# Kernel optimization log

Hardware: AMD Instinct MI355X
Metric: run time of the kernel (lower is better)

## Reference

```python
import jax, jax.numpy as jnp
import numpy as np

N = 8192      # nodes
DIN = 128     # in_channels
DH = 64       # hidden_channels (dim_out, num_heads=1)
DOUT = 32     # out_channels
RATIO = 0.5
K_KEEP = int(np.ceil(RATIO * N))  # SAGPooling keep count (single graph)
LN_EPS = 1e-5


def _linear_params(k, fan_in, fan_out):
    kw, kb = jax.random.split(k)
    W = jax.random.normal(kw, (fan_in, fan_out), dtype=jnp.float32) / jnp.sqrt(jnp.float32(fan_in))
    b = jax.random.normal(kb, (fan_out,), dtype=jnp.float32) * 0.01
    return W, b


def setup_inputs() -> dict:
    key = jax.random.key(0)
    ks = jax.random.split(key, 8)
    x = jax.random.normal(ks[0], (N, DIN), dtype=jnp.float32)
    batch = jnp.zeros((N,), dtype=jnp.int64)  # single graph
    Wq, bq = _linear_params(ks[1], DIN, DH)
    Wk, bk = _linear_params(ks[2], DIN, DH)
    Wv, bv = _linear_params(ks[3], DIN, DH)
    gcn_W, gcn_b = _linear_params(ks[4], DH, DH)       # GCNConv weight/bias
    score_W, score_b = _linear_params(ks[5], DH, 1)    # SAGPooling score GCNConv
    ln_g = jnp.ones((DH,), dtype=jnp.float32)
    ln_b = jnp.zeros((DH,), dtype=jnp.float32)
    head_W, head_b = _linear_params(ks[6], DH, DOUT)
    return dict(x=x, batch=batch, Wq=Wq, bq=bq, Wk=Wk, bk=bk, Wv=Wv, bv=bv,
                gcn_W=gcn_W, gcn_b=gcn_b, score_W=score_W, score_b=score_b,
                ln_g=ln_g, ln_b=ln_b, head_W=head_W, head_b=head_b)


def _forward(x, Wq, bq, Wk, bk, Wv, bv, gcn_W, gcn_b, score_W, score_b,
             ln_g, ln_b, head_W, head_b):
    # --- self-attention over all nodes (num_heads = 1) ---
    Q = x @ Wq + bq                                        # [N, DH]
    K = x @ Wk + bk
    V = x @ Wv + bv
    attn = jax.nn.softmax(Q @ K.T / jnp.sqrt(jnp.float32(DH)), axis=-1)  # [N, N]
    h = attn @ V                                           # [N, DH]

    # --- edge construction: threshold attention, ensure self-loops ---
    # (attn > 0.5).nonzero() -> edge set; empty -> self-loop fallback; then
    # add_self_loops. Dense equivalent: A = max(mask, I).
    eye = jnp.eye(N, dtype=x.dtype)
    A = jnp.maximum((attn > 0.5).astype(x.dtype), eye)     # [N, N], diag = 1

    # symmetric GCN normalization  D^{-1/2} A D^{-1/2}
    dinv = jax.lax.rsqrt(A.sum(axis=1))                    # [N]
    An = dinv[:, None] * A * dinv[None, :]                 # [N, N]

    # --- GCNConv layer ---
    g = An @ (h @ gcn_W) + gcn_b                           # [N, DH]

    # --- SAGPooling: GCNConv scorer -> tanh -> global top-k (single graph) ---
    score = jnp.tanh((An @ (g @ score_W) + score_b).squeeze(-1))  # [N]
    top_scores, perm = jax.lax.top_k(score, K_KEEP)        # sorted desc, like PyG topk
    xp = g[perm] * top_scores[:, None]                     # [K, DH], multiplier = 1

    # --- LayerNorm + ReLU (dropout is identity in eval) ---
    mu = xp.mean(axis=-1, keepdims=True)
    var = xp.var(axis=-1, keepdims=True)
    xp = (xp - mu) * jax.lax.rsqrt(var + LN_EPS) * ln_g + ln_b
    xp = jax.nn.relu(xp)

    # --- prediction head ---
    return xp @ head_W + head_b                            # [K, DOUT]


def reference(x, batch, Wq, bq, Wk, bk, Wv, bv, gcn_W, gcn_b,
              score_W, score_b, ln_g, ln_b, head_W, head_b):
    del batch  # single graph; grouping has no effect on the math
    return _forward(x, Wq, bq, Wk, bk, Wv, bv, gcn_W, gcn_b,
                    score_W, score_b, ln_g, ln_b, head_W, head_b)
```

## Files before the change

kernel.cpp:

```cpp
#include <hip/hip_runtime.h>
#include <hip/hip_bf16.h>
#include <cstdio>

typedef __hip_bfloat16 bf16;
typedef __attribute__((ext_vector_type(8))) short v8s;
typedef __attribute__((ext_vector_type(4))) short v4s;
typedef __attribute__((ext_vector_type(4))) float v4f;
typedef __attribute__((ext_vector_type(4))) double v4d;

#define MFMA16(a, b, c) __builtin_amdgcn_mfma_f32_16x16x32_bf16((a), (b), (c), 0, 0, 0)

#define NN 8192
#define DIN 128
#define DH 64
#define DOUT 32
#define KKEEP 4096
#define SPLITS 16
#define SPATT 16
#define RS2 0.70710678118654752440

__device__ __forceinline__ float bf2f(bf16 v) { return __bfloat162float(v); }
__device__ __forceinline__ short f2bfs(float f) {
  __hip_bfloat16 h = __float2bfloat16(f);
  return *reinterpret_cast<short*>(&h);
}
__device__ __forceinline__ bf16 f2bf(float v) { return __float2bfloat16(v); }

__device__ __forceinline__ double exp_d(double s) {
  const double L2E    = 1.4426950408889634074;
  const double LN2_HI = 6.93147180369123816490e-01;
  const double LN2_LO = 1.90821492927058770002e-10;
  double t  = s * L2E;
  double kf = rint(t);
  double r  = fma(-kf, LN2_HI, s);
  r = fma(-kf, LN2_LO, r);
  double p = 1.0 / 362880.0;
  p = fma(p, r, 1.0 / 40320.0);
  p = fma(p, r, 1.0 / 5040.0);
  p = fma(p, r, 1.0 / 720.0);
  p = fma(p, r, 1.0 / 120.0);
  p = fma(p, r, 1.0 / 24.0);
  p = fma(p, r, 1.0 / 6.0);
  p = fma(p, r, 0.5);
  p = fma(p, r, 1.0);
  p = fma(p, r, 1.0);
  int k = (int)kf;
  long long bits = ((long long)(1023 + k)) << 52;
  double sc = __longlong_as_double(bits);
  return p * sc;
}

__global__ __launch_bounds__(256) void k1_prep(
    const float* __restrict__ x, const float* __restrict__ Wq, const float* __restrict__ bq,
    const float* __restrict__ Wk, const float* __restrict__ bk, const float* __restrict__ Wv,
    const float* __restrict__ bv, const float* __restrict__ gW, const float* __restrict__ sW,
    double* __restrict__ Qd, double* __restrict__ Kd, double* __restrict__ w,
    bf16* __restrict__ Qb, bf16* __restrict__ Kb, bf16* __restrict__ Vt) {
  __shared__ double xs[16][DIN];
  int t = threadIdx.x;
  int nb = blockIdx.x * 16;
  for (int idx = t; idx < 16 * DIN; idx += 256)
    xs[idx >> 7][idx & 127] = (double)x[(size_t)nb * DIN + idx];
  __syncthreads();
  int d = t & 63;
  int sub = t >> 6;
  double ud = 0.0;
  for (int dd = 0; dd < DH; ++dd) ud = fma((double)gW[d * DH + dd], (double)sW[dd], ud);
  double bqd = (double)bq[d];
  double bkd = (double)bk[d];
  double bvd = (double)bv[d];
  for (int pass = 0; pass < 4; ++pass) {
    int n = pass * 4 + sub;
    double aq = bqd, ak = bkd, av = bvd;
#pragma unroll 8
    for (int c = 0; c < DIN; ++c) {
      double xv = xs[n][c];
      aq = fma(xv, (double)Wq[c * DH + d], aq);
      ak = fma(xv, (double)Wk[c * DH + d], ak);
      av = fma(xv, (double)Wv[c * DH + d], av);
    }
    aq *= 0.125;
    int node = nb + n;
    Qd[(size_t)node * DH + d] = aq;
    Kd[(size_t)node * DH + d] = ak;
    Qb[(size_t)node * DH + d] = f2bf((float)aq);
    Kb[(size_t)node * DH + d] = f2bf((float)ak);
    Vt[(size_t)d * NN + node] = f2bf((float)av);
    double pw = av * ud;
#pragma unroll
    for (int off = 32; off; off >>= 1) pw += __shfl_xor(pw, off);
    if (d == 0) w[node] = pw;
  }
}

__global__ __launch_bounds__(256) void k24_seq(
    const double* __restrict__ Qd, const double* __restrict__ Kd, const double* __restrict__ w,
    double* __restrict__ Zp, double* __restrict__ Wp, double* __restrict__ Ep, int* __restrict__ Jp,
    const bf16* __restrict__ Qb, const bf16* __restrict__ Kb, const bf16* __restrict__ Vt,
    float* __restrict__ hp, float* __restrict__ zp) {
  __shared__ __align__(16) char smem[16896];
  const int t = threadIdx.x;
  const int wv = t >> 6;
  const int l = t & 63;

  {
    double (*Kbuf)[16][66] = (double (*)[16][66])smem;
    const int li = l & 15, lg = l >> 4;
    const int rb = (blockIdx.x & 127) * 64;
    const int sp = blockIdx.x >> 7;
    const int cbeg = sp * (NN / SPLITS);

    double qreg[16];
    const double* qrow = Qd + (size_t)(rb + 16 * wv + li) * DH + lg;
#pragma unroll
    for (int tt = 0; tt < 16; ++tt) qreg[tt] = qrow[4 * tt];

    {
      const double* src = Kd + (size_t)cbeg * DH;
      int r = t >> 4, c = (t & 15) * 4;
      *(double2*)&Kbuf[0][r][c]     = *(const double2*)&src[r * DH + c];
      *(double2*)&Kbuf[0][r][c + 2] = *(const double2*)&src[r * DH + c + 2];
    }
    __syncthreads();

    double Zt[4] = {0, 0, 0, 0}, Wt[4] = {0, 0, 0, 0}, Et[4] = {-1, -1, -1, -1};
    int Jt[4] = {0, 0, 0, 0};

    const int NT = (NN / SPLITS) / 16;
    for (int kt = 0; kt < NT; ++kt) {
      const int buf = kt & 1;
      if (kt + 1 < NT) {
        const double* src = Kd + (size_t)(cbeg + (kt + 1) * 16) * DH;
        int r = t >> 4, c = (t & 15) * 4;
        *(double2*)&Kbuf[buf ^ 1][r][c]     = *(const double2*)&src[r * DH + c];
        *(double2*)&Kbuf[buf ^ 1][r][c + 2] = *(const double2*)&src[r * DH + c + 2];
      }
      v4d acc = (v4d){0.0, 0.0, 0.0, 0.0};
      __builtin_amdgcn_s_setprio(1);
#pragma unroll
      for (int tt = 0; tt < 16; ++tt) {
        double bfrag = Kbuf[buf][li][4 * tt + lg];
        acc = __builtin_amdgcn_mfma_f64_16x16x4f64(qreg[tt], bfrag, acc, 0, 0, 0);
      }
      __builtin_amdgcn_s_setprio(0);
      const int col = cbeg + kt * 16 + li;
      const double wj = w[col];
#pragma unroll
      for (int v = 0; v < 4; ++v) {
        double e = exp_d(acc[v]);
        Zt[v] += e;
        Wt[v] = fma(e, wj, Wt[v]);
        if (e > Et[v]) { Et[v] = e; Jt[v] = col; }
      }
      __syncthreads();
    }

#pragma unroll
    for (int v = 0; v < 4; ++v) {
#pragma unroll
      for (int m = 1; m < 16; m <<= 1) {
        Zt[v] += __shfl_xor(Zt[v], m);
        Wt[v] += __shfl_xor(Wt[v], m);
        double e2 = __shfl_xor(Et[v], m);
        int j2 = __shfl_xor(Jt[v], m);
        if (e2 > Et[v] || (e2 == Et[v] && j2 < Jt[v])) { Et[v] = e2; Jt[v] = j2; }
      }
    }
    if (li == 0) {
#pragma unroll
      for (int v = 0; v < 4; ++v) {
        int row = rb + 16 * wv + lg + 4 * v;
        Zp[sp * NN + row] = Zt[v];
        Wp[sp * NN + row] = Wt[v];
        Ep[sp * NN + row] = Et[v];
        Jp[sp * NN + row] = Jt[v];
      }
    }
  }
  __syncthreads();

  {
    short (*P)[16 * 40] = (short (*)[16 * 40])smem;
    const int g = l >> 4, li = l & 15;
    const int qb = (blockIdx.x & 127) * 64 + wv * 16;
    const int sp = blockIdx.x >> 7;
    short* Pw = &P[wv][0];
    const v8s q0 = *(const v8s*)(Qb + (size_t)(qb + li) * DH + g * 8);
    const v8s q1 = *(const v8s*)(Qb + (size_t)(qb + li) * DH + 32 + g * 8);
    v4f hacc[4];
#pragma unroll
    for (int db = 0; db < 4; ++db) hacc[db] = (v4f){0.f, 0.f, 0.f, 0.f};
    float zl = 0.f;
    const int kbeg = sp * (NN / SPATT);
    for (int jb = kbeg; jb < kbeg + NN / SPATT; jb += 32) {
      const bf16* kp = Kb + (size_t)(jb + li) * DH + g * 8;
      v8s ka0 = *(const v8s*)(kp);
      v8s ka1 = *(const v8s*)(kp + 32);
      v8s kb0 = *(const v8s*)(kp + 16 * DH);
      v8s kb1 = *(const v8s*)(kp + 16 * DH + 32);
      v4f c0 = (v4f){0.f, 0.f, 0.f, 0.f}, c1 = (v4f){0.f, 0.f, 0.f, 0.f};
      __builtin_amdgcn_s_setprio(1);
      c0 = MFMA16(ka0, q0, c0);
      c0 = MFMA16(ka1, q1, c0);
      c1 = MFMA16(kb0, q0, c1);
      c1 = MFMA16(kb1, q1, c1);
      __builtin_amdgcn_s_setprio(0);
      v4s p0, p1;
#pragma unroll
      for (int r = 0; r < 4; ++r) {
        short b0 = f2bfs(__expf(c0[r]));
        short b1 = f2bfs(__expf(c1[r]));
        p0[r] = b0;
        p1[r] = b1;
        zl += bf2f(*reinterpret_cast<bf16*>(&b0));
        zl += bf2f(*reinterpret_cast<bf16*>(&b1));
      }
      *(v4s*)&Pw[li * 40 + g * 4] = p0;
      *(v4s*)&Pw[li * 40 + 16 + g * 4] = p1;
      v8s pf = *(const v8s*)&Pw[li * 40 + g * 8];
#pragma unroll
      for (int db = 0; db < 4; ++db) {
        const v8s vb = *(const v8s*)(Vt + (size_t)(db * 16 + li) * NN + jb + g * 8);
        hacc[db] = MFMA16(pf, vb, hacc[db]);
      }
    }
    zl += __shfl_xor(zl, 16);
    zl += __shfl_xor(zl, 32);
    if (g == 0) zp[sp * NN + qb + li] = zl;
#pragma unroll
    for (int r = 0; r < 4; ++r) {
      int row = qb + g * 4 + r;
#pragma unroll
      for (int db = 0; db < 4; ++db)
        hp[((size_t)sp * NN + row) * DH + db * 16 + li] = hacc[db][r];
    }
  }
}

__device__ __forceinline__ double tau_of(int k, const double* __restrict__ Zp,
                                         const double* __restrict__ Wp) {
  double Z = 0, W = 0;
  for (int sp = 0; sp < SPLITS; ++sp) { Z += Zp[sp * NN + k]; W += Wp[sp * NN + k]; }
  return W / Z;
}
__device__ __forceinline__ void exj_of(int k, const double* __restrict__ Zp,
                                       const double* __restrict__ Ep, const int* __restrict__ Jp,
                                       int& exo, int& jo) {
  double Z = 0, E = -1;
  int J = 0;
  for (int sp = 0; sp < SPLITS; ++sp) {
    Z += Zp[sp * NN + k];
    double e = Ep[sp * NN + k];
    if (e > E || (e == E && Jp[sp * NN + k] < J)) { E = e; J = Jp[sp * NN + k]; }
  }
  exo = (E > 0.5 * Z) && (J != k);
  jo = J & (NN - 1);
}
__device__ __forceinline__ double tarr_of(int k, const double* __restrict__ Zp,
                                          const double* __restrict__ Wp,
                                          const double* __restrict__ Ep,
                                          const int* __restrict__ Jp, double cb) {
  int exk, jk;
  exj_of(k, Zp, Ep, Jp, exk, jk);
  double dk = exk ? RS2 : 1.0;
  double acc = dk * tau_of(k, Zp, Wp);
  if (exk) {
    int exj, jj;
    exj_of(jk, Zp, Ep, Jp, exj, jj);
    double dj = exj ? RS2 : 1.0;
    acc = fma(dj, tau_of(jk, Zp, Wp), acc);
  }
  return fma(dk, acc, cb);
}

__global__ void k356(const double* __restrict__ Zp, const double* __restrict__ Wp,
                     const double* __restrict__ Ep, const int* __restrict__ Jp,
                     const float* __restrict__ gb, const float* __restrict__ sW,
                     const float* __restrict__ score_b,
                     int* __restrict__ ex_out, int* __restrict__ jm_out,
                     double* __restrict__ pre, float* __restrict__ sc32, int* __restrict__ cnt) {
  int i = blockIdx.x * 256 + threadIdx.x;
  double cb = 0.0;
  for (int d = 0; d < DH; ++d) cb = fma((double)gb[d], (double)sW[d], cb);
  int exi, ji;
  exj_of(i, Zp, Ep, Jp, exi, ji);
  ex_out[i] = exi;
  jm_out[i] = ji;
  double di = exi ? RS2 : 1.0;
  double acc = di * tarr_of(i, Zp, Wp, Ep, Jp, cb);
  if (exi) {
    int exj, jj;
    exj_of(ji, Zp, Ep, Jp, exj, jj);
    double dj = exj ? RS2 : 1.0;
    acc = fma(dj, tarr_of(ji, Zp, Wp, Ep, Jp, cb), acc);
  }
  double p = fma(di, acc, (double)score_b[0]);
  pre[i] = p;
  sc32[i] = (float)tanh(p);
  cnt[i] = 0;
}

__global__ __launch_bounds__(256) void k9_hM(const float* __restrict__ hp, const float* __restrict__ zp,
                                             const float* __restrict__ gW, float* __restrict__ M) {
  __shared__ float xs[4][DH];
  int t = threadIdx.x;
  int sub = t >> 6, d = t & 63;
  int n = blockIdx.x * 4 + sub;
  float Z = 0.f, H = 0.f;
#pragma unroll
  for (int sp = 0; sp < SPATT; ++sp) {
    Z += zp[sp * NN + n];
    H += hp[((size_t)sp * NN + n) * DH + d];
  }
  xs[sub][d] = H / Z;
  __syncthreads();
  float acc = 0.f;
#pragma unroll 8
  for (int c = 0; c < DH; ++c) acc = fmaf(xs[sub][c], gW[c * DH + d], acc);
  M[(size_t)n * DH + d] = acc;
}

__global__ void k7_rank(const double* __restrict__ pre, int* __restrict__ cnt) {
  __shared__ double pj[512];
  int i = (blockIdx.x & 31) * 256 + threadIdx.x;
  int j0 = (blockIdx.x >> 5) * 512;
  for (int k = threadIdx.x; k < 512; k += 256) pj[k] = pre[j0 + k];
  __syncthreads();
  double si = pre[i];
  int c = 0;
#pragma unroll 8
  for (int j = 0; j < 512; ++j) {
    double v = pj[j];
    c += (v > si || (v == si && (j0 + j) < i));
  }
  atomicAdd(&cnt[i], c);
}

__global__ void k8_sel(const int* __restrict__ cnt, int* __restrict__ sel) {
  int i = blockIdx.x * 256 + threadIdx.x;
  unsigned r = (unsigned)cnt[i];
  if (r < KKEEP) sel[r] = i;
}

__global__ __launch_bounds__(256) void k11_head(const float* __restrict__ M, const int* __restrict__ extra,
                                                const int* __restrict__ jmA, const float* __restrict__ gb,
                                                const float* __restrict__ sc32, const int* __restrict__ sel,
                                                const float* __restrict__ lg, const float* __restrict__ lb,
                                                const float* __restrict__ hW, const float* __restrict__ hb,
                                                float* __restrict__ out) {
  __shared__ float xs[4][DH];
  int t = threadIdx.x;
  int wv = t >> 6, d = t & 63;
  int p = blockIdx.x * 4 + wv;
  int i = sel[p] & (NN - 1);
  int ex = extra[i];
  float di = ex ? 0.70710678f : 1.0f;
  float acc0 = di * M[(size_t)i * DH + d];
  if (ex) {
    int j = jmA[i] & (NN - 1);
    acc0 = fmaf(extra[j] ? 0.70710678f : 1.0f, M[(size_t)j * DH + d], acc0);
  }
  float gval = fmaf(di, acc0, gb[d]);
  float v = gval * sc32[i];
  float s1 = v;
#pragma unroll
  for (int off = 32; off; off >>= 1) s1 += __shfl_xor(s1, off);
  float mu = s1 * (1.0f / 64.0f);
  float dv = v - mu;
  float s2 = dv * dv;
#pragma unroll
  for (int off = 32; off; off >>= 1) s2 += __shfl_xor(s2, off);
  float var = s2 * (1.0f / 64.0f);
  float xn = dv * rsqrtf(var + 1e-5f) * lg[d] + lb[d];
  xs[wv][d] = fmaxf(xn, 0.0f);
  __syncthreads();
  if (t < 128) {
    int r = t >> 5, o = t & 31;
    float acc = hb[o];
#pragma unroll 8
    for (int c = 0; c < DH; ++c) acc = fmaf(xs[r][c], hW[c * DOUT + o], acc);
    out[(size_t)(blockIdx.x * 4 + r) * DOUT + o] = acc;
  }
}

#define MB 1048576ull
constexpr size_t OFF_QD   = 0 * MB;
constexpr size_t OFF_KD   = 4 * MB;
constexpr size_t OFF_M    = 16 * MB;
constexpr size_t OFF_ZP   = 20 * MB;
constexpr size_t OFF_WP   = 21 * MB;
constexpr size_t OFF_EP   = 22 * MB;
constexpr size_t OFF_JP   = 23 * MB;
constexpr size_t OFF_W    = 24 * MB;
constexpr size_t OFF_EX   = 27 * MB;
constexpr size_t OFF_JM   = 28 * MB;
constexpr size_t OFF_PRE  = 30 * MB;
constexpr size_t OFF_SC   = 31 * MB;
constexpr size_t OFF_CNT  = 32 * MB;
constexpr size_t OFF_SEL  = 33 * MB;
constexpr size_t OFF_HP   = 34 * MB;
constexpr size_t OFF_ZATT = 66 * MB;
constexpr size_t OFF_QB   = 67 * MB;
constexpr size_t OFF_KB   = 68 * MB;
constexpr size_t OFF_VT   = 69 * MB;
constexpr size_t WS_NEEDED = 70 * MB;

extern "C" void kernel_launch(void* const* d_in, const int* in_sizes, int n_in,
                              void* d_out, int out_size, void* d_ws, size_t ws_size,
                              hipStream_t stream) {
  if (n_in < 16 || ws_size < WS_NEEDED || out_size != KKEEP * DOUT) {
    fprintf(stderr, "[sag] GUARD ws=%zu need=%zu n_in=%d out=%d\n", ws_size, WS_NEEDED, n_in, out_size);
    return;
  }
  const float* x   = (const float*)d_in[0];
  const float* Wq  = (const float*)d_in[2];
  const float* bq  = (const float*)d_in[3];
  const float* Wk  = (const float*)d_in[4];
  const float* bk  = (const float*)d_in[5];
  const float* Wv  = (const float*)d_in[6];
  const float* bv  = (const float*)d_in[7];
  const float* gW  = (const float*)d_in[8];
  const float* gb  = (const float*)d_in[9];
  const float* sW  = (const float*)d_in[10];
  const float* sb  = (const float*)d_in[11];
  const float* lg  = (const float*)d_in[12];
  const float* lb  = (const float*)d_in[13];
  const float* hW  = (const float*)d_in[14];
  const float* hb  = (const float*)d_in[15];
  float* out = (float*)d_out;

  char* ws = (char*)d_ws;
  double* Qd  = (double*)(ws + OFF_QD);
  double* Kd  = (double*)(ws + OFF_KD);
  bf16*   Qb  = (bf16*)(ws + OFF_QB);
  bf16*   Kb  = (bf16*)(ws + OFF_KB);
  bf16*   Vt  = (bf16*)(ws + OFF_VT);
  float*  M   = (float*)(ws + OFF_M);
  double* Zp  = (double*)(ws + OFF_ZP);
  double* Wp  = (double*)(ws + OFF_WP);
  double* Ep  = (double*)(ws + OFF_EP);
  int*    Jp  = (int*)(ws + OFF_JP);
  double* w   = (double*)(ws + OFF_W);
  int*    ex  = (int*)(ws + OFF_EX);
  int*    jm  = (int*)(ws + OFF_JM);
  double* pre = (double*)(ws + OFF_PRE);
  float*  sc32= (float*)(ws + OFF_SC);
  int*    cnt = (int*)(ws + OFF_CNT);
  int*    sel = (int*)(ws + OFF_SEL);
  float*  hp  = (float*)(ws + OFF_HP);
  float*  zatt= (float*)(ws + OFF_ZATT);

  hipLaunchKernelGGL(k1_prep, dim3(512), dim3(256), 0, stream, x, Wq, bq, Wk, bk, Wv, bv,
                     gW, sW, Qd, Kd, w, Qb, Kb, Vt);
  hipLaunchKernelGGL(k24_seq, dim3(128 * SPLITS), dim3(256), 0, stream,
                     Qd, Kd, w, Zp, Wp, Ep, Jp, Qb, Kb, Vt, hp, zatt);
  hipLaunchKernelGGL(k9_hM, dim3(2048), dim3(256), 0, stream, hp, zatt, gW, M);
  hipLaunchKernelGGL(k356, dim3(32), dim3(256), 0, stream, Zp, Wp, Ep, Jp, gb, sW, sb,
                     ex, jm, pre, sc32, cnt);
  hipLaunchKernelGGL(k7_rank, dim3(512), dim3(256), 0, stream, pre, cnt);
  hipLaunchKernelGGL(k8_sel, dim3(32), dim3(256), 0, stream, cnt, sel);
  hipLaunchKernelGGL(k11_head, dim3(1024), dim3(256), 0, stream, M, ex, jm, gb, sc32, sel,
                     lg, lb, hW, hb, out);
}
```

Before: 348.9 us.

## Fuse tail kernels into one cooperative kernel with grid syncs

Replaces the five tail launches (hM projection, score, rank, select, head) with a single cooperative kernel that uses grid.sync between phases. The aim is to remove per-launch overhead and the idle gaps between small dependent kernels. If the cooperative launch fails, it falls back to the original sequence. A grid-wide barrier costs something each time, and the 1024 blocks must all be co-resident.

```diff
diff --git a/kernel.cpp b/kernel.cpp
--- a/kernel.cpp
+++ b/kernel.cpp
@@ -1,6 +1,9 @@
 #include <hip/hip_runtime.h>
 #include <hip/hip_bf16.h>
+#include <hip/hip_cooperative_groups.h>
 #include <cstdio>
+
+namespace cg = cooperative_groups;
 
 typedef __hip_bfloat16 bf16;
 typedef __attribute__((ext_vector_type(8))) short v8s;
@@ -273,13 +276,11 @@
   return fma(dk, acc, cb);
 }
 
-__global__ void k356(const double* __restrict__ Zp, const double* __restrict__ Wp,
-                     const double* __restrict__ Ep, const int* __restrict__ Jp,
-                     const float* __restrict__ gb, const float* __restrict__ sW,
-                     const float* __restrict__ score_b,
-                     int* __restrict__ ex_out, int* __restrict__ jm_out,
-                     double* __restrict__ pre, float* __restrict__ sc32, int* __restrict__ cnt) {
-  int i = blockIdx.x * 256 + threadIdx.x;
+__device__ __forceinline__ void k356_body(int i, const double* Zp, const double* Wp,
+                                          const double* Ep, const int* Jp, const float* gb,
+                                          const float* sW, const float* score_b,
+                                          int* ex_out, int* jm_out, double* pre,
+                                          float* sc32, int* cnt) {
   double cb = 0.0;
   for (int d = 0; d < DH; ++d) cb = fma((double)gb[d], (double)sW[d], cb);
   int exi, ji;
@@ -298,6 +299,113 @@
   pre[i] = p;
   sc32[i] = (float)tanh(p);
   cnt[i] = 0;
+}
+
+__global__ __launch_bounds__(256) void k_tail(
+    const float* __restrict__ hp, const float* __restrict__ zp, const float* __restrict__ gW,
+    float* __restrict__ M,
+    const double* __restrict__ Zp, const double* __restrict__ Wp,
+    const double* __restrict__ Ep, const int* __restrict__ Jp,
+    const float* __restrict__ gb, const float* __restrict__ sW, const float* __restrict__ sb,
+    int* __restrict__ ex, int* __restrict__ jm, double* __restrict__ pre,
+    float* __restrict__ sc32, int* __restrict__ cnt, int* __restrict__ sel,
+    const float* __restrict__ lg, const float* __restrict__ lb,
+    const float* __restrict__ hW, const float* __restrict__ hb, float* __restrict__ out) {
+  cg::grid_group grid = cg::this_grid();
+  __shared__ __align__(16) char smem[2048];
+  const int t = threadIdx.x, bid = blockIdx.x;
+
+  {
+    float (*xs)[DH] = (float (*)[DH])smem;
+    int sub = t >> 6, d = t & 63;
+    for (int sw = 0; sw < 2; ++sw) {
+      int n = sw * 4096 + bid * 4 + sub;
+      float Z = 0.f, H = 0.f;
+#pragma unroll
+      for (int sp = 0; sp < SPATT; ++sp) {
+        Z += zp[sp * NN + n];
+        H += hp[((size_t)sp * NN + n) * DH + d];
+      }
+      xs[sub][d] = H / Z;
+      __syncthreads();
+      float acc = 0.f;
+#pragma unroll 8
+      for (int c = 0; c < DH; ++c) acc = fmaf(xs[sub][c], gW[c * DH + d], acc);
+      M[(size_t)n * DH + d] = acc;
+      __syncthreads();
+    }
+  }
+  if (bid < 32) k356_body(bid * 256 + t, Zp, Wp, Ep, Jp, gb, sW, sb, ex, jm, pre, sc32, cnt);
+  grid.sync();
+
+  {
+    double* pj = (double*)smem;
+    int i = (bid & 31) * 256 + t;
+    int j0 = (bid >> 5) * 256;
+    pj[t] = pre[j0 + t];
+    __syncthreads();
+    double si = pre[i];
+    int c = 0;
+#pragma unroll 8
+    for (int j = 0; j < 256; ++j) {
+      double v = pj[j];
+      c += (v > si || (v == si && (j0 + j) < i));
+    }
+    atomicAdd(&cnt[i], c);
+  }
+  grid.sync();
+
+  if (bid < 32) {
+    int i = bid * 256 + t;
+    unsigned r = (unsigned)cnt[i];
+    if (r < KKEEP) sel[r] = i;
+  }
+  grid.sync();
+
+  {
+    float (*xs)[DH] = (float (*)[DH])smem;
+    int wv = t >> 6, d = t & 63;
+    int p = bid * 4 + wv;
+    int i = sel[p] & (NN - 1);
+    int exi = ex[i];
+    float di = exi ? 0.70710678f : 1.0f;
+    float acc0 = di * M[(size_t)i * DH + d];
+    if (exi) {
+      int j = jm[i] & (NN - 1);
+      acc0 = fmaf(ex[j] ? 0.70710678f : 1.0f, M[(size_t)j * DH + d], acc0);
+    }
+    float gval = fmaf(di, acc0, gb[d]);
+    float v = gval * sc32[i];
+    float s1 = v;
+#pragma unroll
+    for (int off = 32; off; off >>= 1) s1 += __shfl_xor(s1, off);
+    float mu = s1 * (1.0f / 64.0f);
+    float dv = v - mu;
+    float s2 = dv * dv;
+#pragma unroll
+    for (int off = 32; off; off >>= 1) s2 += __shfl_xor(s2, off);
+    float var = s2 * (1.0f / 64.0f);
+    float xn = dv * rsqrtf(var + 1e-5f) * lg[d] + lb[d];
+    xs[wv][d] = fmaxf(xn, 0.0f);
+    __syncthreads();
+    if (t < 128) {
+      int r = t >> 5, o = t & 31;
+      float acc = hb[o];
+#pragma unroll 8
+      for (int c = 0; c < DH; ++c) acc = fmaf(xs[r][c], hW[c * DOUT + o], acc);
+      out[(size_t)(bid * 4 + r) * DOUT + o] = acc;
+    }
+  }
+}
+
+__global__ void k356(const double* __restrict__ Zp, const double* __restrict__ Wp,
+                     const double* __restrict__ Ep, const int* __restrict__ Jp,
+                     const float* __restrict__ gb, const float* __restrict__ sW,
+                     const float* __restrict__ score_b,
+                     int* __restrict__ ex_out, int* __restrict__ jm_out,
+                     double* __restrict__ pre, float* __restrict__ sc32, int* __restrict__ cnt) {
+  int i = blockIdx.x * 256 + threadIdx.x;
+  k356_body(i, Zp, Wp, Ep, Jp, gb, sW, score_b, ex_out, jm_out, pre, sc32, cnt);
 }
 
 __global__ __launch_bounds__(256) void k9_hM(const float* __restrict__ hp, const float* __restrict__ zp,
@@ -454,11 +562,18 @@
                      gW, sW, Qd, Kd, w, Qb, Kb, Vt);
   hipLaunchKernelGGL(k24_seq, dim3(128 * SPLITS), dim3(256), 0, stream,
                      Qd, Kd, w, Zp, Wp, Ep, Jp, Qb, Kb, Vt, hp, zatt);
-  hipLaunchKernelGGL(k9_hM, dim3(2048), dim3(256), 0, stream, hp, zatt, gW, M);
-  hipLaunchKernelGGL(k356, dim3(32), dim3(256), 0, stream, Zp, Wp, Ep, Jp, gb, sW, sb,
-                     ex, jm, pre, sc32, cnt);
-  hipLaunchKernelGGL(k7_rank, dim3(512), dim3(256), 0, stream, pre, cnt);
-  hipLaunchKernelGGL(k8_sel, dim3(32), dim3(256), 0, stream, cnt, sel);
-  hipLaunchKernelGGL(k11_head, dim3(1024), dim3(256), 0, stream, M, ex, jm, gb, sc32, sel,
-                     lg, lb, hW, hb, out);
-}
+
+  void* kargs[] = {&hp, &zatt, &gW, &M, &Zp, &Wp, &Ep, &Jp, &gb, &sW, &sb,
+                   &ex, &jm, &pre, &sc32, &cnt, &sel, &lg, &lb, &hW, &hb, &out};
+  hipError_t ce = hipLaunchCooperativeKernel((const void*)k_tail, dim3(1024), dim3(256),
+                                             kargs, 0, stream);
+  if (ce != hipSuccess) {
+    hipLaunchKernelGGL(k9_hM, dim3(2048), dim3(256), 0, stream, hp, zatt, gW, M);
+    hipLaunchKernelGGL(k356, dim3(32), dim3(256), 0, stream, Zp, Wp, Ep, Jp, gb, sW, sb,
+                       ex, jm, pre, sc32, cnt);
+    hipLaunchKernelGGL(k7_rank, dim3(512), dim3(256), 0, stream, pre, cnt);
+    hipLaunchKernelGGL(k8_sel, dim3(32), dim3(256), 0, stream, cnt, sel);
+    hipLaunchKernelGGL(k11_head, dim3(1024), dim3(256), 0, stream, M, ex, jm, gb, sc32, sel,
+                       lg, lb, hW, hb, out);
+  }
+}
```

After: 648.1 us. 1.86x slower.
